# Performance work log

Hardware: AMD Instinct MI355X
Metric: run time of the kernel (lower is better)

The kernel has to match this reference:

```python
import jax, jax.numpy as jnp
import numpy as np

N = 50000      # num nodes
E = 1_200_000  # num edges
NID = 92       # node_input_dim
ED = 1         # edge_input_dim
H = 64         # hidden_dim
L = 5          # num_layers
EMB = 64       # embedding_dim
G = 256        # num graphs in batch
EPS = 1e-5


def _glorot(key, shape):
    fan_in, fan_out = shape[-2], shape[-1]
    lim = float(np.sqrt(6.0 / (fan_in + fan_out)))
    return jax.random.uniform(key, shape, jnp.float32, -lim, lim)


def setup_inputs() -> dict:
    key = jax.random.key(0)
    ks = jax.random.split(key, 16)
    inp = {
        "x": jax.random.normal(ks[0], (N, NID), jnp.float32),
        "edge_attr": jax.random.uniform(ks[1], (E, ED), jnp.float32),
        "edge_index": jax.random.randint(ks[2], (2, E), 0, N, jnp.int32),
        "batch": jnp.sort(jax.random.randint(ks[3], (N,), 0, G, jnp.int32)),
        # node embedding
        "node_W": _glorot(ks[4], (NID, H)),
        "node_b": jnp.zeros((H,), jnp.float32),
        # per-layer message net: Linear(2H+ED,H) -> BN -> SiLU -> Linear(H,H)
        "msg_W1": _glorot(ks[5], (L, 2 * H + ED, H)),
        "msg_b1": jnp.zeros((L, H), jnp.float32),
        "msg_g1": jnp.ones((L, H), jnp.float32),
        "msg_be1": jnp.zeros((L, H), jnp.float32),
        "msg_W2": _glorot(ks[6], (L, H, H)),
        "msg_b2": jnp.zeros((L, H), jnp.float32),
        # per-layer update net: Linear(2H,H) -> BN -> SiLU
        "upd_W": _glorot(ks[7], (L, 2 * H, H)),
        "upd_b": jnp.zeros((L, H), jnp.float32),
        "upd_g": jnp.ones((L, H), jnp.float32),
        "upd_be": jnp.zeros((L, H), jnp.float32),
        # output projection
        "out_W": _glorot(ks[8], (H, EMB)),
        "out_b": jnp.zeros((EMB,), jnp.float32),
    }
    return inp


def _bn(z, g, b):
    # BatchNorm1d, training-mode batch statistics (biased variance), eps=1e-5
    mu = jnp.mean(z, axis=0)
    var = jnp.var(z, axis=0)
    return (z - mu) * jax.lax.rsqrt(var + EPS) * g + b


def reference(x, edge_attr, node_W, node_b, msg_W1, msg_b1, msg_g1, msg_be1,
              msg_W2, msg_b2, upd_W, upd_b, upd_g, upd_be, out_W, out_b,
              edge_index, batch):
    src, dst = edge_index[0], edge_index[1]  # PyG: x_j = x[src], x_i = x[dst]
    h = x @ node_W + node_b                  # [N, H]
    deg = jax.ops.segment_sum(jnp.ones((E,), h.dtype), dst, num_segments=N)
    deg = jnp.maximum(deg, 1.0)[:, None]     # mean aggregation denominator
    for l in range(L):
        # message: cat([x_i, x_j, edge_attr]) -> Linear -> BN -> SiLU -> Linear
        m = jnp.concatenate([h[dst], h[src], edge_attr], axis=1)  # [E, 2H+ED]
        m = _bn(m @ msg_W1[l] + msg_b1[l], msg_g1[l], msg_be1[l])
        m = jax.nn.silu(m) @ msg_W2[l] + msg_b2[l]                # [E, H]
        # aggregate: scatter-mean to destination nodes
        agg = jax.ops.segment_sum(m, dst, num_segments=N) / deg   # [N, H]
        # update: cat([x, agg]) -> Linear -> BN -> SiLU
        u = jnp.concatenate([h, agg], axis=1) @ upd_W[l] + upd_b[l]
        h = jax.nn.silu(_bn(u, upd_g[l], upd_be[l]))              # [N, H]
    # global mean pool over graphs
    cnt = jnp.maximum(jax.ops.segment_sum(jnp.ones((N,), h.dtype), batch, num_segments=G), 1.0)
    g = jax.ops.segment_sum(h, batch, num_segments=G) / cnt[:, None]  # [G, H]
    return jax.nn.silu(g @ out_W + out_b)                              # [G, EMB]
```

## Files before the change

### kernel.cpp

```cpp
#include <hip/hip_runtime.h>
#include <hip/hip_bf16.h>

#define NN 50000
#define EE 1200000
#define GG 256
#define LL 5

__device__ __forceinline__ float silu_f(float x) {
    return x * __builtin_amdgcn_rcpf(1.0f + __expf(-x));
}
__device__ __forceinline__ int rfl(int x) { return __builtin_amdgcn_readfirstlane(x); }

__global__ __launch_bounds__(256) void k_hist(const int* __restrict__ ei, int* __restrict__ fill, int E) {
    int e = blockIdx.x * 256 + threadIdx.x;
    if (e < E) atomicAdd(&fill[ei[E + e]], 1);
}

__global__ __launch_bounds__(256) void k_scan_blk(int* __restrict__ fill, int* __restrict__ rowptr,
                                                  float* __restrict__ degf, int* __restrict__ bsum, int n) {
    __shared__ int wsum[4];
    int tid = threadIdx.x, lane = tid & 63, wid = tid >> 6;
    int i = blockIdx.x * 256 + tid;
    int v = (i < n) ? fill[i] : 0;
    int x = v;
    #pragma unroll
    for (int off = 1; off < 64; off <<= 1) {
        int t = __shfl_up(x, off);
        if (lane >= off) x += t;
    }
    if (lane == 63) wsum[wid] = x;
    __syncthreads();
    int waveoff = 0;
    if (wid > 0) waveoff += wsum[0];
    if (wid > 1) waveoff += wsum[1];
    if (wid > 2) waveoff += wsum[2];
    int inc = x + waveoff;
    if (i < n) {
        rowptr[i + 1] = inc;
        degf[i] = (float)(v > 0 ? v : 1);
        fill[i] = 0;
    }
    if (tid == 255) bsum[blockIdx.x] = inc;
}

__global__ __launch_bounds__(256) void k_scan_top(int* __restrict__ bsum, int B) {
    __shared__ int wsum[4];
    int tid = threadIdx.x, lane = tid & 63, wid = tid >> 6;
    int v = (tid < B) ? bsum[tid] : 0;
    int x = v;
    #pragma unroll
    for (int off = 1; off < 64; off <<= 1) {
        int t = __shfl_up(x, off);
        if (lane >= off) x += t;
    }
    if (lane == 63) wsum[wid] = x;
    __syncthreads();
    int waveoff = 0;
    if (wid > 0) waveoff += wsum[0];
    if (wid > 1) waveoff += wsum[1];
    if (wid > 2) waveoff += wsum[2];
    if (tid < B) bsum[tid] = x + waveoff;
}

__global__ __launch_bounds__(256) void k_scan_add(const int* __restrict__ bsum, int* __restrict__ rowptr, int n) {
    int b = blockIdx.x;
    int i = b * 256 + threadIdx.x;
    if (i < n) {
        int add = (b > 0) ? bsum[b - 1] : 0;
        rowptr[i + 1] += add;
    }
    if (i == 0) rowptr[0] = 0;
}

__global__ __launch_bounds__(256) void k_scatter(const int* __restrict__ ei, const float* __restrict__ ea,
                                                 const int* __restrict__ rowptr, int* __restrict__ fill,
                                                 unsigned int* __restrict__ edata, int E) {
    int e = blockIdx.x * 256 + threadIdx.x;
    if (e < E) {
        int d = ei[E + e];
        int pos = atomicAdd(&fill[d], 1);
        int idx = rowptr[d] + pos;
        int ea15 = (int)(ea[e] * 32768.0f + 0.5f);
        if (ea15 > 32767) ea15 = 32767;
        edata[idx] = ((unsigned int)ea15 << 17) | (unsigned int)ei[e];
    }
}

__global__ __launch_bounds__(256) void k_fold(const float* __restrict__ msg_W2, const float* __restrict__ msg_b2,
                                              const float* __restrict__ upd_W, float* __restrict__ W2p,
                                              float* __restrict__ b2p) {
    int l = blockIdx.x;
    const float* W2 = msg_W2 + (size_t)l * 4096;
    const float* U2 = upd_W + (size_t)l * 8192 + 4096;
    int lane = threadIdx.x & 63, wid = threadIdx.x >> 6;
    for (int ii = 0; ii < 16; ii++) {
        int i = rfl(wid * 16 + ii);
        float acc = 0.0f;
        for (int k = 0; k < 64; k++) acc = fmaf(W2[i * 64 + k], U2[k * 64 + lane], acc);
        W2p[(size_t)l * 4096 + i * 64 + lane] = acc;
    }
    if (wid == 0) {
        float acc = 0.0f;
        for (int k = 0; k < 64; k++) acc = fmaf(msg_b2[l * 64 + k], U2[k * 64 + lane], acc);
        b2p[l * 64 + lane] = acc;
    }
}

__global__ __launch_bounds__(256) void k_node_emb(const float* __restrict__ x, const float* __restrict__ W,
                                                  const float* __restrict__ b, float* __restrict__ h, int n) {
    __shared__ float sW[92 * 64];
    __shared__ float sX[4][736];
    for (int i = threadIdx.x; i < 92 * 64; i += 256) sW[i] = W[i];
    __syncthreads();
    int lane = threadIdx.x & 63, wid = threadIdx.x >> 6;
    int gw = (blockIdx.x * 256 + threadIdx.x) >> 6;
    int nw = (gridDim.x * 256) >> 6;
    float bj = b[lane];
    int tiles = n >> 3;
    for (int t = gw; t < tiles; t += nw) {
        int rb = rfl(t << 3);
        const float4* xb = (const float4*)(x + (size_t)rb * 92);
        float4* sx4 = (float4*)&sX[wid][0];
        sx4[lane] = xb[lane];
        sx4[lane + 64] = xb[lane + 64];
        if (lane < 56) sx4[lane + 128] = xb[lane + 128];
        float acc[8];
        #pragma unroll
        for (int r = 0; r < 8; r++) acc[r] = bj;
        for (int kb = 0; kb < 80; kb += 16) {
            float wv[16];
            #pragma unroll
            for (int t2 = 0; t2 < 16; t2++) wv[t2] = sW[(kb + t2) * 64 + lane];
            #pragma unroll
            for (int r = 0; r < 8; r++) {
                #pragma unroll
                for (int t2 = 0; t2 < 16; t2++) acc[r] = fmaf(sX[wid][r * 92 + kb + t2], wv[t2], acc[r]);
            }
        }
        {
            float wv[12];
            #pragma unroll
            for (int t2 = 0; t2 < 12; t2++) wv[t2] = sW[(80 + t2) * 64 + lane];
            #pragma unroll
            for (int r = 0; r < 8; r++) {
                #pragma unroll
                for (int t2 = 0; t2 < 12; t2++) acc[r] = fmaf(sX[wid][r * 92 + 80 + t2], wv[t2], acc[r]);
            }
        }
        #pragma unroll
        for (int r = 0; r < 8; r++) h[(size_t)(rb + r) * 64 + lane] = acc[r];
    }
}

__global__ __launch_bounds__(256) void k_node_pre(const float* __restrict__ h, const float* __restrict__ W1,
                                                  const float* __restrict__ b1, float* __restrict__ Hd,
                                                  _Float16* __restrict__ Hs, int n) {
    __shared__ float sA[4096], sB[4096];
    __shared__ float sH[4][512];
    for (int i = threadIdx.x; i < 4096; i += 256) { sA[i] = W1[i]; sB[i] = W1[4096 + i]; }
    __syncthreads();
    int lane = threadIdx.x & 63, wid = threadIdx.x >> 6;
    int gw = (blockIdx.x * 256 + threadIdx.x) >> 6;
    int nw = (gridDim.x * 256) >> 6;
    float bj = b1[lane];
    int tiles = n >> 3;
    for (int t = gw; t < tiles; t += nw) {
        int rb = rfl(t << 3);
        const float4* hb = (const float4*)(h + (size_t)rb * 64);
        float4* sh4 = (float4*)&sH[wid][0];
        sh4[lane] = hb[lane];
        sh4[lane + 64] = hb[lane + 64];
        float accA[8], accB[8];
        #pragma unroll
        for (int r = 0; r < 8; r++) { accA[r] = bj; accB[r] = 0.0f; }
        for (int kb = 0; kb < 64; kb += 8) {
            float wA[8], wB[8];
            #pragma unroll
            for (int t2 = 0; t2 < 8; t2++) { wA[t2] = sA[(kb + t2) * 64 + lane]; wB[t2] = sB[(kb + t2) * 64 + lane]; }
            #pragma unroll
            for (int r = 0; r < 8; r++) {
                #pragma unroll
                for (int t2 = 0; t2 < 8; t2++) {
                    float hk = sH[wid][r * 64 + kb + t2];
                    accA[r] = fmaf(hk, wA[t2], accA[r]);
                    accB[r] = fmaf(hk, wB[t2], accB[r]);
                }
            }
        }
        #pragma unroll
        for (int r = 0; r < 8; r++) {
            Hd[(size_t)(rb + r) * 64 + lane] = accA[r];
            Hs[(size_t)(rb + r) * 64 + lane] = (_Float16)accB[r];
        }
    }
}

__global__ __launch_bounds__(256) void k_bn_pre(const float* __restrict__ u, const float* __restrict__ usum,
                                                const float* __restrict__ usq, const float* __restrict__ g,
                                                const float* __restrict__ be, const float* __restrict__ W1,
                                                const float* __restrict__ b1, float* __restrict__ h,
                                                float* __restrict__ Hd, _Float16* __restrict__ Hs,
                                                int n, float invN) {
    __shared__ float sA[4096], sB[4096];
    __shared__ float sH[4][8][64];
    for (int i = threadIdx.x; i < 4096; i += 256) { sA[i] = W1[i]; sB[i] = W1[4096 + i]; }
    __syncthreads();
    int lane = threadIdx.x & 63, wid = threadIdx.x >> 6;
    float mean = usum[lane] * invN;
    float var = usq[lane] * invN - mean * mean;
    float inv = rsqrtf(var + 1e-5f);
    float sc = inv * g[lane];
    float sh = fmaf(-mean, sc, be[lane]);
    float bj = b1[lane];
    int gw = (blockIdx.x * 256 + threadIdx.x) >> 6;
    int nw = (gridDim.x * 256) >> 6;
    int tiles = n >> 3;
    for (int t = gw; t < tiles; t += nw) {
        int rb = rfl(t << 3);
        #pragma unroll
        for (int r = 0; r < 8; r++) {
            float uv = u[(size_t)(rb + r) * 64 + lane];
            float hv = silu_f(fmaf(uv, sc, sh));
            h[(size_t)(rb + r) * 64 + lane] = hv;
            sH[wid][r][lane] = hv;
        }
        float accA[8], accB[8];
        #pragma unroll
        for (int r = 0; r < 8; r++) { accA[r] = bj; accB[r] = 0.0f; }
        for (int k = 0; k < 64; k += 2) {
            float wA0 = sA[k * 64 + lane],       wB0 = sB[k * 64 + lane];
            float wA1 = sA[(k + 1) * 64 + lane], wB1 = sB[(k + 1) * 64 + lane];
            #pragma unroll
            for (int r = 0; r < 8; r++) {
                float h0 = sH[wid][r][k], h1 = sH[wid][r][k + 1];
                accA[r] = fmaf(h0, wA0, accA[r]);
                accB[r] = fmaf(h0, wB0, accB[r]);
                accA[r] = fmaf(h1, wA1, accA[r]);
                accB[r] = fmaf(h1, wB1, accB[r]);
            }
        }
        #pragma unroll
        for (int r = 0; r < 8; r++) {
            Hd[(size_t)(rb + r) * 64 + lane] = accA[r];
            Hs[(size_t)(rb + r) * 64 + lane] = (_Float16)accB[r];
        }
    }
}

__global__ __launch_bounds__(256) void k_edge_stats(const float* __restrict__ Hd, const _Float16* __restrict__ Hs,
                                                    const int* __restrict__ rowptr, const unsigned int* __restrict__ edata,
                                                    const float* __restrict__ w1e,
                                                    float* __restrict__ esum, float* __restrict__ esq, int n) {
    __shared__ float rs[4][64], rq[4][64];
    int wid = threadIdx.x >> 6, lane = threadIdx.x & 63;
    int gw = (blockIdx.x * 256 + threadIdx.x) >> 6;
    int nw = (gridDim.x * 256) >> 6;
    float wj = w1e[lane] * (1.0f / 32768.0f);
    float s = 0.0f, q = 0.0f;
    for (int node = gw; node < n; node += nw) {
        int nu = rfl(node);
        int e0 = rfl(rowptr[nu]), e1 = rfl(rowptr[nu + 1]);
        if (e0 == e1) continue;
        float hd = Hd[(size_t)nu * 64 + lane];
        int nc = (e1 - e0) >> 3;
        int e = e0 + (nc << 3);
        if (nc > 0) {
            unsigned int pc[8];
            #pragma unroll
            for (int j = 0; j < 8; j++) pc[j] = edata[e0 + j];
            int eb = e0 + 8;
            for (int c = 0; c < nc - 1; c++, eb += 8) {
                float hs[8], av[8];
                #pragma unroll
                for (int j = 0; j < 8; j++) {
                    int sidx = rfl((int)(pc[j] & 0x1FFFFu));
                    av[j] = (float)rfl((int)(pc[j] >> 17));
                    hs[j] = (float)Hs[(size_t)sidx * 64 + lane];
                }
                #pragma unroll
                for (int j = 0; j < 8; j++) pc[j] = edata[eb + j];
                #pragma unroll
                for (int j = 0; j < 8; j++) {
                    float z = fmaf(av[j], wj, hd) + hs[j];
                    s += z;
                    q = fmaf(z, z, q);
                }
            }
            {
                float hs[8], av[8];
                #pragma unroll
                for (int j = 0; j < 8; j++) {
                    int sidx = rfl((int)(pc[j] & 0x1FFFFu));
                    av[j] = (float)rfl((int)(pc[j] >> 17));
                    hs[j] = (float)Hs[(size_t)sidx * 64 + lane];
                }
                #pragma unroll
                for (int j = 0; j < 8; j++) {
                    float z = fmaf(av[j], wj, hd) + hs[j];
                    s += z;
                    q = fmaf(z, z, q);
                }
            }
        }
        for (; e < e1; e++) {
            unsigned int p = edata[e];
            int sidx = rfl((int)(p & 0x1FFFFu));
            float a = (float)rfl((int)(p >> 17));
            float z = fmaf(a, wj, hd) + (float)Hs[(size_t)sidx * 64 + lane];
            s += z;
            q = fmaf(z, z, q);
        }
    }
    rs[wid][lane] = s; rq[wid][lane] = q;
    __syncthreads();
    if (wid == 0) {
        float ts = rs[0][lane] + rs[1][lane] + rs[2][lane] + rs[3][lane];
        float tq = rq[0][lane] + rq[1][lane] + rq[2][lane] + rq[3][lane];
        atomicAdd(&esum[lane], ts);
        atomicAdd(&esq[lane], tq);
    }
}

__global__ __launch_bounds__(256) void k_agg_upd(const float* __restrict__ Hd, const _Float16* __restrict__ Hs,
                                                 const int* __restrict__ rowptr, const unsigned int* __restrict__ edata,
                                                 const float* __restrict__ w1e,
                                                 const float* __restrict__ esum, const float* __restrict__ esq,
                                                 const float* __restrict__ g1, const float* __restrict__ be1,
                                                 const float* __restrict__ degf,
                                                 const float* __restrict__ h, const float* __restrict__ U1,
                                                 const float* __restrict__ W2p, const float* __restrict__ b2p,
                                                 const float* __restrict__ ub,
                                                 float* __restrict__ u, float* __restrict__ usum,
                                                 float* __restrict__ usq, int n, float invE) {
    __shared__ float sU[4096], sP[4096];
    __shared__ float2 sHA[4][4][64];
    for (int i = threadIdx.x; i < 4096; i += 256) { sU[i] = U1[i]; sP[i] = W2p[i]; }
    __syncthreads();
    int lane = threadIdx.x & 63, wid = threadIdx.x >> 6;
    float mean = esum[lane] * invE;
    float var = esq[lane] * invE - mean * mean;
    float inv = rsqrtf(var + 1e-5f);
    float sc = inv * g1[lane];
    float sh = fmaf(-mean, sc, be1[lane]);
    float wj = w1e[lane] * (1.0f / 32768.0f);
    float b2j = b2p[lane], ubj = ub[lane];
    int gw = (blockIdx.x * 256 + threadIdx.x) >> 6;
    int nw = (gridDim.x * 256) >> 6;
    float s = 0.0f, q = 0.0f;
    int tiles = n >> 2;
    for (int t = gw; t < tiles; t += nw) {
        int rb = rfl(t << 2);
        float gate[4];
        for (int r = 0; r < 4; r++) {
            int nu = rb + r;
            int e0 = rfl(rowptr[nu]), e1 = rfl(rowptr[nu + 1]);
            gate[r] = (e1 > e0) ? 1.0f : 0.0f;
            float hd = Hd[(size_t)nu * 64 + lane];
            float hvv = h[(size_t)nu * 64 + lane];
            float acc = 0.0f;
            int nc = (e1 - e0) >> 3;
            int e = e0 + (nc << 3);
            if (nc > 0) {
                unsigned int pc[8];
                #pragma unroll
                for (int j = 0; j < 8; j++) pc[j] = edata[e0 + j];
                int eb = e0 + 8;
                for (int c = 0; c < nc - 1; c++, eb += 8) {
                    float hs[8], av[8];
                    #pragma unroll
                    for (int j = 0; j < 8; j++) {
                        int sidx = rfl((int)(pc[j] & 0x1FFFFu));
                        av[j] = (float)rfl((int)(pc[j] >> 17));
                        hs[j] = (float)Hs[(size_t)sidx * 64 + lane];
                    }
                    #pragma unroll
                    for (int j = 0; j < 8; j++) pc[j] = edata[eb + j];
                    #pragma unroll
                    for (int j = 0; j < 8; j++) {
                        float z = fmaf(av[j], wj, hd) + hs[j];
                        acc += silu_f(fmaf(z, sc, sh));
                    }
                }
                {
                    float hs[8], av[8];
                    #pragma unroll
                    for (int j = 0; j < 8; j++) {
                        int sidx = rfl((int)(pc[j] & 0x1FFFFu));
                        av[j] = (float)rfl((int)(pc[j] >> 17));
                        hs[j] = (float)Hs[(size_t)sidx * 64 + lane];
                    }
                    #pragma unroll
                    for (int j = 0; j < 8; j++) {
                        float z = fmaf(av[j], wj, hd) + hs[j];
                        acc += silu_f(fmaf(z, sc, sh));
                    }
                }
            }
            for (; e < e1; e++) {
                unsigned int p = edata[e];
                int sidx = rfl((int)(p & 0x1FFFFu));
                float a = (float)rfl((int)(p >> 17));
                float z = fmaf(a, wj, hd) + (float)Hs[(size_t)sidx * 64 + lane];
                acc += silu_f(fmaf(z, sc, sh));
            }
            sHA[wid][r][lane] = make_float2(hvv, acc / degf[nu]);
        }
        float accu[4];
        #pragma unroll
        for (int r = 0; r < 4; r++) accu[r] = fmaf(gate[r], b2j, ubj);
        for (int k = 0; k < 64; k++) {
            float wU = sU[k * 64 + lane], wP = sP[k * 64 + lane];
            #pragma unroll
            for (int r = 0; r < 4; r++) {
                float2 ha = sHA[wid][r][k];
                accu[r] = fmaf(ha.x, wU, accu[r]);
                accu[r] = fmaf(ha.y, wP, accu[r]);
            }
        }
        #pragma unroll
        for (int r = 0; r < 4; r++) {
            u[(size_t)(rb + r) * 64 + lane] = accu[r];
            s += accu[r];
            q = fmaf(accu[r], accu[r], q);
        }
    }
    {
        float* my = (float*)&sHA[wid][0][0];
        my[lane] = s;
        my[64 + lane] = q;
    }
    __syncthreads();
    if (wid == 0) {
        float ts = 0.0f, tq = 0.0f;
        #pragma unroll
        for (int w = 0; w < 4; w++) {
            const float* b = (const float*)&sHA[w][0][0];
            ts += b[lane];
            tq += b[64 + lane];
        }
        atomicAdd(&usum[lane], ts);
        atomicAdd(&usq[lane], tq);
    }
}

__global__ __launch_bounds__(256) void k_bn_pool(const float* __restrict__ u, const float* __restrict__ usum,
                                                 const float* __restrict__ usq, const float* __restrict__ g,
                                                 const float* __restrict__ be, const int* __restrict__ batch,
                                                 float* __restrict__ gsum, float* __restrict__ gcnt,
                                                 int n, float invN) {
    __shared__ float ssc[64], ssh[64];
    if (threadIdx.x < 64) {
        int j = threadIdx.x;
        float mean = usum[j] * invN;
        float var = usq[j] * invN - mean * mean;
        float inv = rsqrtf(var + 1e-5f);
        float sc = inv * g[j];
        ssc[j] = sc;
        ssh[j] = fmaf(-mean, sc, be[j]);
    }
    __syncthreads();
    int lane = threadIdx.x & 63;
    int gw = (blockIdx.x * 256 + threadIdx.x) >> 6;
    int nw = (gridDim.x * 256) >> 6;
    int per = (n + nw - 1) / nw;
    int start = gw * per;
    int end = start + per; if (end > n) end = n;
    if (start >= end) return;
    float sc = ssc[lane], sh = ssh[lane];
    int cur = batch[start];
    float acc = 0.0f, c = 0.0f;
    for (int i = start; i < end; i++) {
        int b = batch[i];
        if (b != cur) {
            atomicAdd(&gsum[(size_t)cur * 64 + lane], acc);
            if (lane == 0) atomicAdd(&gcnt[cur], c);
            cur = b; acc = 0.0f; c = 0.0f;
        }
        float y = fmaf(u[(size_t)i * 64 + lane], sc, sh);
        acc += silu_f(y);
        c += 1.0f;
    }
    atomicAdd(&gsum[(size_t)cur * 64 + lane], acc);
    if (lane == 0) atomicAdd(&gcnt[cur], c);
}

__global__ __launch_bounds__(256) void k_out(const float* __restrict__ gsum, const float* __restrict__ gcnt,
                                             const float* __restrict__ OW, const float* __restrict__ ob,
                                             float* __restrict__ out, int G) {
    __shared__ float sW[4096];
    for (int i = threadIdx.x; i < 4096; i += 256) sW[i] = OW[i];
    __syncthreads();
    int lane = threadIdx.x & 63;
    int gw = (blockIdx.x * 256 + threadIdx.x) >> 6;
    int nw = (gridDim.x * 256) >> 6;
    for (int g = gw; g < G; g += nw) {
        int gu = rfl(g);
        float c = gcnt[gu]; if (c < 1.0f) c = 1.0f;
        float ci = 1.0f / c;
        float acc = ob[lane];
        const float* gr = gsum + (size_t)gu * 64;
        #pragma unroll
        for (int k = 0; k < 64; k++) acc = fmaf(gr[k] * ci, sW[k * 64 + lane], acc);
        out[(size_t)gu * 64 + lane] = silu_f(acc);
    }
}

extern "C" void kernel_launch(void* const* d_in, const int* in_sizes, int n_in,
                              void* d_out, int out_size, void* d_ws, size_t ws_size,
                              hipStream_t stream) {
    const int N = NN, E = EE, G = GG, L = LL;
    const float* x         = (const float*)d_in[0];
    const float* edge_attr = (const float*)d_in[1];
    const int*   edge_index= (const int*)d_in[2];
    const int*   batch     = (const int*)d_in[3];
    const float* node_W    = (const float*)d_in[4];
    const float* node_b    = (const float*)d_in[5];
    const float* msg_W1    = (const float*)d_in[6];
    const float* msg_b1    = (const float*)d_in[7];
    const float* msg_g1    = (const float*)d_in[8];
    const float* msg_be1   = (const float*)d_in[9];
    const float* msg_W2    = (const float*)d_in[10];
    const float* msg_b2    = (const float*)d_in[11];
    const float* upd_W     = (const float*)d_in[12];
    const float* upd_b     = (const float*)d_in[13];
    const float* upd_g     = (const float*)d_in[14];
    const float* upd_be    = (const float*)d_in[15];
    const float* out_W     = (const float*)d_in[16];
    const float* out_b     = (const float*)d_in[17];
    float* out = (float*)d_out;

    char* ws = (char*)d_ws;
    size_t off = 0;
    auto alloc = [&](size_t b) { size_t o = off; off = (off + b + 255) & ~(size_t)255; return o; };
    float* h    = (float*)(ws + alloc((size_t)N * 64 * 4));
    float* Hd   = (float*)(ws + alloc((size_t)N * 64 * 4));
    _Float16* Hs = (_Float16*)(ws + alloc((size_t)N * 64 * 2));
    unsigned int* edata = (unsigned int*)(ws + alloc((size_t)E * 4));
    int* rowptr = (int*)  (ws + alloc((size_t)(N + 1) * 4));
    float* degf = (float*)(ws + alloc((size_t)N * 4));
    float* W2p  = (float*)(ws + alloc((size_t)L * 4096 * 4));
    float* b2p  = (float*)(ws + alloc((size_t)L * 64 * 4));
    int* bsum   = (int*)  (ws + alloc((size_t)256 * 4));
    size_t zero_begin = off;
    int*   fill = (int*)  (ws + alloc((size_t)N * 4));
    float* stats= (float*)(ws + alloc((size_t)L * 4 * 64 * 4));
    float* gsum = (float*)(ws + alloc((size_t)(G * 64 + G) * 4));
    size_t zero_end = off;
    float* gcnt = gsum + (size_t)G * 64;
    float* u = Hd;

    hipMemsetAsync(ws + zero_begin, 0, zero_end - zero_begin, stream);

    const int SB = (N + 255) / 256;
    k_hist<<<(E + 255) / 256, 256, 0, stream>>>(edge_index, fill, E);
    k_scan_blk<<<SB, 256, 0, stream>>>(fill, rowptr, degf, bsum, N);
    k_scan_top<<<1, 256, 0, stream>>>(bsum, SB);
    k_scan_add<<<SB, 256, 0, stream>>>(bsum, rowptr, N);
    k_scatter<<<(E + 255) / 256, 256, 0, stream>>>(edge_index, edge_attr, rowptr, fill, edata, E);

    k_fold<<<L, 256, 0, stream>>>(msg_W2, msg_b2, upd_W, W2p, b2p);
    k_node_emb<<<1024, 256, 0, stream>>>(x, node_W, node_b, h, N);

    k_node_pre<<<1024, 256, 0, stream>>>(h, msg_W1, msg_b1, Hd, Hs, N);

    for (int l = 0; l < L; l++) {
        const float* W1  = msg_W1 + (size_t)l * 129 * 64;
        const float* w1e = W1 + 128 * 64;
        float* esum = stats + (size_t)l * 256;
        float* esq  = esum + 64;
        float* usum = esum + 128;
        float* usq  = esum + 192;
        k_edge_stats<<<2048, 256, 0, stream>>>(Hd, Hs, rowptr, edata, w1e, esum, esq, N);
        k_agg_upd<<<1024, 256, 0, stream>>>(Hd, Hs, rowptr, edata, w1e, esum, esq,
                                            msg_g1 + l * 64, msg_be1 + l * 64, degf,
                                            h, upd_W + (size_t)l * 8192, W2p + (size_t)l * 4096,
                                            b2p + (size_t)l * 64, upd_b + l * 64,
                                            u, usum, usq, N, 1.0f / E);
        if (l < L - 1) {
            const float* W1n = msg_W1 + (size_t)(l + 1) * 129 * 64;
            k_bn_pre<<<1024, 256, 0, stream>>>(u, usum, usq, upd_g + l * 64, upd_be + l * 64,
                                               W1n, msg_b1 + (l + 1) * 64, h, Hd, Hs, N, 1.0f / N);
        } else {
            k_bn_pool<<<256, 256, 0, stream>>>(u, usum, usq, upd_g + l * 64, upd_be + l * 64,
                                               batch, gsum, gcnt, N, 1.0f / N);
        }
    }

    k_out<<<64, 256, 0, stream>>>(gsum, gcnt, out_W, out_b, out, G);
}
```

Measured before the change: 1.169 ms.

## Split fused edge aggregation and node update into separate kernels

The fused aggregate-plus-update kernel becomes two kernels. The edge gather/SiLU aggregation now runs without large shared-memory matrices, one node per wave at higher occupancy, and writes mean-aggregated messages to a new buffer. A second kernel performs the node-update GEMV, tiling 8 nodes per wave. The CSR build also records each edge's position from the histogram atomic so the scatter pass needs no second atomic, uses nontemporal stores, and edge_stats grid size is doubled. This costs an extra N×64 float round trip through memory and an extra launch per layer.

```diff
diff --git a/kernel.cpp b/kernel.cpp
--- a/kernel.cpp
+++ b/kernel.cpp
@@ -11,9 +11,10 @@
 }
 __device__ __forceinline__ int rfl(int x) { return __builtin_amdgcn_readfirstlane(x); }
 
-__global__ __launch_bounds__(256) void k_hist(const int* __restrict__ ei, int* __restrict__ fill, int E) {
+__global__ __launch_bounds__(256) void k_hist(const int* __restrict__ ei, int* __restrict__ fill,
+                                              int* __restrict__ posb, int E) {
     int e = blockIdx.x * 256 + threadIdx.x;
-    if (e < E) atomicAdd(&fill[ei[E + e]], 1);
+    if (e < E) posb[e] = atomicAdd(&fill[ei[E + e]], 1);
 }
 
 __global__ __launch_bounds__(256) void k_scan_blk(int* __restrict__ fill, int* __restrict__ rowptr,
@@ -38,7 +39,6 @@
     if (i < n) {
         rowptr[i + 1] = inc;
         degf[i] = (float)(v > 0 ? v : 1);
-        fill[i] = 0;
     }
     if (tid == 255) bsum[blockIdx.x] = inc;
 }
@@ -73,16 +73,16 @@
 }
 
 __global__ __launch_bounds__(256) void k_scatter(const int* __restrict__ ei, const float* __restrict__ ea,
-                                                 const int* __restrict__ rowptr, int* __restrict__ fill,
+                                                 const int* __restrict__ rowptr, const int* __restrict__ posb,
                                                  unsigned int* __restrict__ edata, int E) {
     int e = blockIdx.x * 256 + threadIdx.x;
     if (e < E) {
         int d = ei[E + e];
-        int pos = atomicAdd(&fill[d], 1);
-        int idx = rowptr[d] + pos;
+        int idx = rowptr[d] + posb[e];
         int ea15 = (int)(ea[e] * 32768.0f + 0.5f);
         if (ea15 > 32767) ea15 = 32767;
-        edata[idx] = ((unsigned int)ea15 << 17) | (unsigned int)ei[e];
+        unsigned int v = ((unsigned int)ea15 << 17) | (unsigned int)ei[e];
+        __builtin_nontemporal_store(v, &edata[idx]);
     }
 }
 
@@ -321,123 +321,127 @@
     }
 }
 
-__global__ __launch_bounds__(256) void k_agg_upd(const float* __restrict__ Hd, const _Float16* __restrict__ Hs,
-                                                 const int* __restrict__ rowptr, const unsigned int* __restrict__ edata,
-                                                 const float* __restrict__ w1e,
-                                                 const float* __restrict__ esum, const float* __restrict__ esq,
-                                                 const float* __restrict__ g1, const float* __restrict__ be1,
-                                                 const float* __restrict__ degf,
-                                                 const float* __restrict__ h, const float* __restrict__ U1,
-                                                 const float* __restrict__ W2p, const float* __restrict__ b2p,
-                                                 const float* __restrict__ ub,
-                                                 float* __restrict__ u, float* __restrict__ usum,
-                                                 float* __restrict__ usq, int n, float invE) {
-    __shared__ float sU[4096], sP[4096];
-    __shared__ float2 sHA[4][4][64];
-    for (int i = threadIdx.x; i < 4096; i += 256) { sU[i] = U1[i]; sP[i] = W2p[i]; }
-    __syncthreads();
-    int lane = threadIdx.x & 63, wid = threadIdx.x >> 6;
+__global__ __launch_bounds__(256, 8) void k_edge_agg(const float* __restrict__ Hd, const _Float16* __restrict__ Hs,
+                                                     const int* __restrict__ rowptr, const unsigned int* __restrict__ edata,
+                                                     const float* __restrict__ w1e,
+                                                     const float* __restrict__ esum, const float* __restrict__ esq,
+                                                     const float* __restrict__ g1, const float* __restrict__ be1,
+                                                     const float* __restrict__ degf, float* __restrict__ sacc,
+                                                     int n, float invE) {
+    int lane = threadIdx.x & 63;
     float mean = esum[lane] * invE;
     float var = esq[lane] * invE - mean * mean;
     float inv = rsqrtf(var + 1e-5f);
     float sc = inv * g1[lane];
     float sh = fmaf(-mean, sc, be1[lane]);
     float wj = w1e[lane] * (1.0f / 32768.0f);
+    int gw = (blockIdx.x * 256 + threadIdx.x) >> 6;
+    int nw = (gridDim.x * 256) >> 6;
+    for (int node = gw; node < n; node += nw) {
+        int nu = rfl(node);
+        int e0 = rfl(rowptr[nu]), e1 = rfl(rowptr[nu + 1]);
+        float hd = Hd[(size_t)nu * 64 + lane];
+        float acc = 0.0f;
+        int nc = (e1 - e0) >> 3;
+        int e = e0 + (nc << 3);
+        if (nc > 0) {
+            unsigned int pc[8];
+            #pragma unroll
+            for (int j = 0; j < 8; j++) pc[j] = edata[e0 + j];
+            int eb = e0 + 8;
+            for (int c = 0; c < nc - 1; c++, eb += 8) {
+                float hs[8], av[8];
+                #pragma unroll
+                for (int j = 0; j < 8; j++) {
+                    int sidx = rfl((int)(pc[j] & 0x1FFFFu));
+                    av[j] = (float)rfl((int)(pc[j] >> 17));
+                    hs[j] = (float)Hs[(size_t)sidx * 64 + lane];
+                }
+                #pragma unroll
+                for (int j = 0; j < 8; j++) pc[j] = edata[eb + j];
+                #pragma unroll
+                for (int j = 0; j < 8; j++) {
+                    float z = fmaf(av[j], wj, hd) + hs[j];
+                    acc += silu_f(fmaf(z, sc, sh));
+                }
+            }
+            {
+                float hs[8], av[8];
+                #pragma unroll
+                for (int j = 0; j < 8; j++) {
+                    int sidx = rfl((int)(pc[j] & 0x1FFFFu));
+                    av[j] = (float)rfl((int)(pc[j] >> 17));
+                    hs[j] = (float)Hs[(size_t)sidx * 64 + lane];
+                }
+                #pragma unroll
+                for (int j = 0; j < 8; j++) {
+                    float z = fmaf(av[j], wj, hd) + hs[j];
+                    acc += silu_f(fmaf(z, sc, sh));
+                }
+            }
+        }
+        for (; e < e1; e++) {
+            unsigned int p = edata[e];
+            int sidx = rfl((int)(p & 0x1FFFFu));
+            float a = (float)rfl((int)(p >> 17));
+            float z = fmaf(a, wj, hd) + (float)Hs[(size_t)sidx * 64 + lane];
+            acc += silu_f(fmaf(z, sc, sh));
+        }
+        sacc[(size_t)nu * 64 + lane] = acc / degf[nu];
+    }
+}
+
+__global__ __launch_bounds__(256) void k_node_upd(const float* __restrict__ h, const float* __restrict__ sacc,
+                                                  const int* __restrict__ rowptr,
+                                                  const float* __restrict__ U1, const float* __restrict__ W2p,
+                                                  const float* __restrict__ b2p, const float* __restrict__ ub,
+                                                  float* __restrict__ u, float* __restrict__ usum,
+                                                  float* __restrict__ usq, int n) {
+    __shared__ float sU[4096], sP[4096];
+    __shared__ float2 sHA[4][8][64];
+    __shared__ float rs[4][64], rq[4][64];
+    for (int i = threadIdx.x; i < 4096; i += 256) { sU[i] = U1[i]; sP[i] = W2p[i]; }
+    __syncthreads();
+    int lane = threadIdx.x & 63, wid = threadIdx.x >> 6;
     float b2j = b2p[lane], ubj = ub[lane];
     int gw = (blockIdx.x * 256 + threadIdx.x) >> 6;
     int nw = (gridDim.x * 256) >> 6;
     float s = 0.0f, q = 0.0f;
-    int tiles = n >> 2;
+    int tiles = n >> 3;
     for (int t = gw; t < tiles; t += nw) {
-        int rb = rfl(t << 2);
-        float gate[4];
-        for (int r = 0; r < 4; r++) {
-            int nu = rb + r;
-            int e0 = rfl(rowptr[nu]), e1 = rfl(rowptr[nu + 1]);
-            gate[r] = (e1 > e0) ? 1.0f : 0.0f;
-            float hd = Hd[(size_t)nu * 64 + lane];
-            float hvv = h[(size_t)nu * 64 + lane];
-            float acc = 0.0f;
-            int nc = (e1 - e0) >> 3;
-            int e = e0 + (nc << 3);
-            if (nc > 0) {
-                unsigned int pc[8];
-                #pragma unroll
-                for (int j = 0; j < 8; j++) pc[j] = edata[e0 + j];
-                int eb = e0 + 8;
-                for (int c = 0; c < nc - 1; c++, eb += 8) {
-                    float hs[8], av[8];
-                    #pragma unroll
-                    for (int j = 0; j < 8; j++) {
-                        int sidx = rfl((int)(pc[j] & 0x1FFFFu));
-                        av[j] = (float)rfl((int)(pc[j] >> 17));
-                        hs[j] = (float)Hs[(size_t)sidx * 64 + lane];
-                    }
-                    #pragma unroll
-                    for (int j = 0; j < 8; j++) pc[j] = edata[eb + j];
-                    #pragma unroll
-                    for (int j = 0; j < 8; j++) {
-                        float z = fmaf(av[j], wj, hd) + hs[j];
-                        acc += silu_f(fmaf(z, sc, sh));
-                    }
-                }
-                {
-                    float hs[8], av[8];
-                    #pragma unroll
-                    for (int j = 0; j < 8; j++) {
-                        int sidx = rfl((int)(pc[j] & 0x1FFFFu));
-                        av[j] = (float)rfl((int)(pc[j] >> 17));
-                        hs[j] = (float)Hs[(size_t)sidx * 64 + lane];
-                    }
-                    #pragma unroll
-                    for (int j = 0; j < 8; j++) {
-                        float z = fmaf(av[j], wj, hd) + hs[j];
-                        acc += silu_f(fmaf(z, sc, sh));
-                    }
-                }
-            }
-            for (; e < e1; e++) {
-                unsigned int p = edata[e];
-                int sidx = rfl((int)(p & 0x1FFFFu));
-                float a = (float)rfl((int)(p >> 17));
-                float z = fmaf(a, wj, hd) + (float)Hs[(size_t)sidx * 64 + lane];
-                acc += silu_f(fmaf(z, sc, sh));
-            }
-            sHA[wid][r][lane] = make_float2(hvv, acc / degf[nu]);
-        }
-        float accu[4];
-        #pragma unroll
-        for (int r = 0; r < 4; r++) accu[r] = fmaf(gate[r], b2j, ubj);
+        int rb = rfl(t << 3);
+        #pragma unroll
+        for (int r = 0; r < 8; r++) {
+            sHA[wid][r][lane] = make_float2(h[(size_t)(rb + r) * 64 + lane],
+                                            sacc[(size_t)(rb + r) * 64 + lane]);
+        }
+        float accu[8];
+        #pragma unroll
+        for (int r = 0; r < 8; r++) {
+            int c0 = rowptr[rb + r], c1 = rowptr[rb + r + 1];
+            accu[r] = fmaf((c1 > c0) ? 1.0f : 0.0f, b2j, ubj);
+        }
         for (int k = 0; k < 64; k++) {
             float wU = sU[k * 64 + lane], wP = sP[k * 64 + lane];
             #pragma unroll
-            for (int r = 0; r < 4; r++) {
+            for (int r = 0; r < 8; r++) {
                 float2 ha = sHA[wid][r][k];
                 accu[r] = fmaf(ha.x, wU, accu[r]);
                 accu[r] = fmaf(ha.y, wP, accu[r]);
             }
         }
         #pragma unroll
-        for (int r = 0; r < 4; r++) {
+        for (int r = 0; r < 8; r++) {
             u[(size_t)(rb + r) * 64 + lane] = accu[r];
             s += accu[r];
             q = fmaf(accu[r], accu[r], q);
         }
     }
-    {
-        float* my = (float*)&sHA[wid][0][0];
-        my[lane] = s;
-        my[64 + lane] = q;
-    }
+    rs[wid][lane] = s; rq[wid][lane] = q;
     __syncthreads();
     if (wid == 0) {
-        float ts = 0.0f, tq = 0.0f;
-        #pragma unroll
-        for (int w = 0; w < 4; w++) {
-            const float* b = (const float*)&sHA[w][0][0];
-            ts += b[lane];
-            tq += b[64 + lane];
-        }
+        float ts = rs[0][lane] + rs[1][lane] + rs[2][lane] + rs[3][lane];
+        float tq = rq[0][lane] + rq[1][lane] + rq[2][lane] + rq[3][lane];
         atomicAdd(&usum[lane], ts);
         atomicAdd(&usq[lane], tq);
     }
@@ -535,7 +539,9 @@
     float* h    = (float*)(ws + alloc((size_t)N * 64 * 4));
     float* Hd   = (float*)(ws + alloc((size_t)N * 64 * 4));
     _Float16* Hs = (_Float16*)(ws + alloc((size_t)N * 64 * 2));
+    float* sacc = (float*)(ws + alloc((size_t)N * 64 * 4));
     unsigned int* edata = (unsigned int*)(ws + alloc((size_t)E * 4));
+    int* posb   = (int*)  (ws + alloc((size_t)E * 4));
     int* rowptr = (int*)  (ws + alloc((size_t)(N + 1) * 4));
     float* degf = (float*)(ws + alloc((size_t)N * 4));
     float* W2p  = (float*)(ws + alloc((size_t)L * 4096 * 4));
@@ -552,11 +558,11 @@
     hipMemsetAsync(ws + zero_begin, 0, zero_end - zero_begin, stream);
 
     const int SB = (N + 255) / 256;
-    k_hist<<<(E + 255) / 256, 256, 0, stream>>>(edge_index, fill, E);
+    k_hist<<<(E + 255) / 256, 256, 0, stream>>>(edge_index, fill, posb, E);
     k_scan_blk<<<SB, 256, 0, stream>>>(fill, rowptr, degf, bsum, N);
     k_scan_top<<<1, 256, 0, stream>>>(bsum, SB);
     k_scan_add<<<SB, 256, 0, stream>>>(bsum, rowptr, N);
-    k_scatter<<<(E + 255) / 256, 256, 0, stream>>>(edge_index, edge_attr, rowptr, fill, edata, E);
+    k_scatter<<<(E + 255) / 256, 256, 0, stream>>>(edge_index, edge_attr, rowptr, posb, edata, E);
 
     k_fold<<<L, 256, 0, stream>>>(msg_W2, msg_b2, upd_W, W2p, b2p);
     k_node_emb<<<1024, 256, 0, stream>>>(x, node_W, node_b, h, N);
@@ -570,12 +576,12 @@
         float* esq  = esum + 64;
         float* usum = esum + 128;
         float* usq  = esum + 192;
-        k_edge_stats<<<2048, 256, 0, stream>>>(Hd, Hs, rowptr, edata, w1e, esum, esq, N);
-        k_agg_upd<<<1024, 256, 0, stream>>>(Hd, Hs, rowptr, edata, w1e, esum, esq,
-                                            msg_g1 + l * 64, msg_be1 + l * 64, degf,
-                                            h, upd_W + (size_t)l * 8192, W2p + (size_t)l * 4096,
-                                            b2p + (size_t)l * 64, upd_b + l * 64,
-                                            u, usum, usq, N, 1.0f / E);
+        k_edge_stats<<<4096, 256, 0, stream>>>(Hd, Hs, rowptr, edata, w1e, esum, esq, N);
+        k_edge_agg<<<2048, 256, 0, stream>>>(Hd, Hs, rowptr, edata, w1e, esum, esq,
+                                             msg_g1 + l * 64, msg_be1 + l * 64, degf, sacc, N, 1.0f / E);
+        k_node_upd<<<1024, 256, 0, stream>>>(h, sacc, rowptr, upd_W + (size_t)l * 8192,
+                                             W2p + (size_t)l * 4096, b2p + (size_t)l * 64, upd_b + l * 64,
+                                             u, usum, usq, N);
         if (l < L - 1) {
             const float* W1n = msg_W1 + (size_t)(l + 1) * 129 * 64;
             k_bn_pre<<<1024, 256, 0, stream>>>(u, usum, usq, upd_g + l * 64, upd_be + l * 64,
```

After: 1.377 ms. +17.7%, slower.
